# Optimization experiments

Hardware: AMD Instinct MI355X
Metric: run time of the kernel (lower is better)

## Reference

```python
import jax, jax.numpy as jnp
import numpy as np

N = 30000      # nodes
IN = 768       # input feature dim
C = 128        # hidden channels (= conv out_dim, = gate dim)
HEADS = 4      # attention heads (TransformerConv and Semantic)
DH = 128       # per-head dim (concat=False -> out_channels)
R = 3          # num relations
E = 80000      # edges per relation
NEG = 0.01     # LeakyReLU slope


def setup_inputs() -> dict:
    key = jax.random.key(0)
    ks = iter(jax.random.split(key, 64))
    def nx(shape):
        return jax.random.normal(next(ks), shape, dtype=jnp.float32) * 0.02
    inp = {}
    inp["x"] = jax.random.normal(next(ks), (N, IN), dtype=jnp.float32)
    inp["edges"] = jax.random.randint(next(ks), (R, 2, E), 0, N, dtype=jnp.int32)
    inp["lin1_W"] = nx((IN, C)); inp["lin1_b"] = jnp.zeros((C,), jnp.float32)
    for l in ("l1", "l2"):
        inp[f"{l}_Wq"] = nx((R, C, HEADS * DH)); inp[f"{l}_bq"] = jnp.zeros((R, HEADS * DH), jnp.float32)
        inp[f"{l}_Wk"] = nx((R, C, HEADS * DH)); inp[f"{l}_bk"] = jnp.zeros((R, HEADS * DH), jnp.float32)
        inp[f"{l}_Wv"] = nx((R, C, HEADS * DH)); inp[f"{l}_bv"] = jnp.zeros((R, HEADS * DH), jnp.float32)
        inp[f"{l}_Ws"] = nx((R, C, DH));         inp[f"{l}_bs"] = jnp.zeros((R, DH), jnp.float32)
        inp[f"{l}_gW"] = nx((C + DH, C));        inp[f"{l}_gb"] = jnp.zeros((C,), jnp.float32)
        inp[f"{l}_sW1"] = nx((HEADS, C, C));     inp[f"{l}_sb1"] = jnp.zeros((HEADS, C), jnp.float32)
        inp[f"{l}_sw2"] = nx((HEADS, C))
    inp["lin2_W"] = nx((C, C)); inp["lin2_b"] = jnp.zeros((C,), jnp.float32)
    inp["clf_W"] = nx((C, 2)); inp["clf_b"] = jnp.zeros((2,), jnp.float32)
    return inp


def lrelu(x):
    return jnp.where(x >= 0, x, NEG * x)


def transformer_conv(x, src, dst, Wq, bq, Wk, bk, Wv, bv, Ws, bs):
    # PyG TransformerConv, heads=HEADS, concat=False (head mean), root_weight=True, eval (no dropout)
    n = x.shape[0]
    q = (x @ Wq + bq).reshape(n, HEADS, DH)
    k = (x @ Wk + bk).reshape(n, HEADS, DH)
    v = (x @ Wv + bv).reshape(n, HEADS, DH)
    logits = (q[dst] * k[src]).sum(-1) / np.sqrt(DH)      # [E, H]
    m = jax.ops.segment_max(logits, dst, num_segments=n)  # scatter-softmax (stable)
    a = jnp.exp(logits - m[dst])
    s = jax.ops.segment_sum(a, dst, num_segments=n)
    alpha = a / s[dst]
    agg = jax.ops.segment_sum(alpha[:, :, None] * v[src], dst, num_segments=n)  # [N, H, DH]
    return agg.mean(axis=1) + x @ Ws + bs


def semantic(Hm, sW1, sb1, sw2):
    # Hm: [N, R, C]; per-head scoring MLP -> softmax over relations -> weighted sum, averaged over heads
    t = jnp.tanh(jnp.einsum('nrc,hco->hnro', Hm, sW1) + sb1[:, None, None, :])  # [H, N, R, C]
    scores = jnp.einsum('hnro,ho->hnr', t, sw2).mean(axis=1)                    # [H, R]
    beta = jax.nn.softmax(scores, axis=-1)
    return jnp.einsum('hr,nrc->nc', beta, Hm) / HEADS


def rgt_layer(x, edges, Wq, bq, Wk, bk, Wv, bv, Ws, bs, gW, gb, sW1, sb1, sw2):
    Hs = []
    for r in range(R):  # small fixed relation loop
        src, dst = edges[r, 0], edges[r, 1]
        U = transformer_conv(x, src, dst, Wq[r], bq[r], Wk[r], bk[r], Wv[r], bv[r], Ws[r], bs[r])
        Z = jax.nn.sigmoid(jnp.concatenate([U, x], axis=1) @ gW + gb)
        Hs.append(jnp.tanh(U) * Z + x * (1.0 - Z))
    Hm = jnp.stack(Hs, axis=1)  # [N, R, C]
    return semantic(Hm, sW1, sb1, sw2)


def reference(x, edges, lin1_W, lin1_b,
              l1_Wq, l1_bq, l1_Wk, l1_bk, l1_Wv, l1_bv, l1_Ws, l1_bs, l1_gW, l1_gb, l1_sW1, l1_sb1, l1_sw2,
              l2_Wq, l2_bq, l2_Wk, l2_bk, l2_Wv, l2_bv, l2_Ws, l2_bs, l2_gW, l2_gb, l2_sW1, l2_sb1, l2_sw2,
              lin2_W, lin2_b, clf_W, clf_b):
    h = lrelu(x @ lin1_W + lin1_b)
    h = rgt_layer(h, edges, l1_Wq, l1_bq, l1_Wk, l1_bk, l1_Wv, l1_bv, l1_Ws, l1_bs, l1_gW, l1_gb, l1_sW1, l1_sb1, l1_sw2)
    h = rgt_layer(h, edges, l2_Wq, l2_bq, l2_Wk, l2_bk, l2_Wv, l2_bv, l2_Ws, l2_bs, l2_gW, l2_gb, l2_sW1, l2_sb1, l2_sw2)
    h = lrelu(h @ lin2_W + lin2_b)
    return h @ clf_W + clf_b
```

## Files before the change

kernel.cpp:

```cpp
#include <hip/hip_runtime.h>
#include <math.h>

#define Nn 30000
#define RR 3
#define EE 80000
#define MT_M 235

#define SAP 72
#define EP_LD 68
#define AS3 136
#define KBIG 0x40000000

typedef __attribute__((ext_vector_type(8))) short bf16x8;
typedef __attribute__((ext_vector_type(4))) float f32x4;

__device__ __forceinline__ unsigned short f2bf(float f) {
    union { float f; unsigned u; } v; v.f = f;
    unsigned r = v.u + 0x7fff + ((v.u >> 16) & 1);
    return (unsigned short)(r >> 16);
}
__device__ __forceinline__ float bf2f(short h) {
    union { unsigned u; float f; } v;
    v.u = ((unsigned)(unsigned short)h) << 16;
    return v.f;
// ... 28 lines not shown
    const int wave = t >> 6;
    const int wm = (wave >> 1) << 6;
    const int wn = (wave & 1) << 6;
    const int fr = lane & 15;
    const int quad = lane >> 4;

    for (int k0 = 0; k0 < K; k0 += 64) {
        const short* Abase; int kk0, ldax;
        if (k0 < ksplit) { Abase = A;  kk0 = k0;          ldax = lda;  }
        else             { Abase = A2; kk0 = k0 - ksplit; ldax = lda2; }
        #pragma unroll
        for (int rr = 0; rr < 4; rr++) {
            int r = srow + rr * 32;
            int gr = m0 + r;
            bf16x8 va = {0, 0, 0, 0, 0, 0, 0, 0};
            if (gr < M) va = *(const bf16x8*)(Abase + (size_t)gr * ldax + kk0 + scol);
            *(bf16x8*)(As + r * SAP + scol) = va;
        }
        #pragma unroll
        for (int rr = 0; rr < 4; rr++) {
            int r = srow + rr * 32;
            bf16x8 vb = *(const bf16x8*)(Bt + (size_t)(n0 + r) * K + k0 + scol);
            *(bf16x8*)(Bs + r * SAP + scol) = vb;
        }
        __syncthreads();
        #pragma unroll
        for (int kc = 0; kc < 2; kc++) {
            bf16x8 af[4], bfr[4];
            #pragma unroll
            for (int i = 0; i < 4; i++)
                af[i] = *(const bf16x8*)(As + (wm + i * 16 + fr) * SAP + kc * 32 + quad * 8);
            #pragma unroll
            for (int i = 0; i < 4; i++)
                bfr[i] = *(const bf16x8*)(Bs + (wn + i * 16 + fr) * SAP + kc * 32 + quad * 8);
            #pragma unroll
            for (int mi = 0; mi < 4; mi++)
                #pragma unroll
                for (int ni = 0; ni < 4; ni++)
                    acc[mi][ni] = __builtin_amdgcn_mfma_f32_16x16x32_bf16(
                        af[mi], bfr[ni], acc[mi][ni], 0, 0, 0);
        }
        __syncthreads();
    }
}

__global__ __launch_bounds__(256) void gemm_mfma(
    const short* __restrict__ A, int lda,
    const short* __restrict__ A2, int lda2, int ksplit,
    const short* __restrict__ Bt, const float* __restrict__ bias,
    float* __restrict__ C, int ldc, short* __restrict__ Cbf, int ldcbf,
    int M, int K, int act)
{
    __shared__ short As[128 * SAP];
    __shared__ short Bs[128 * SAP];
    f32x4 acc[4][4];
    #pragma unroll
    for (int i = 0; i < 4; i++)
        #pragma unroll
        for (int j = 0; j < 4; j++) acc[i][j] = (f32x4){0.f, 0.f, 0.f, 0.f};
    int m0 = blockIdx.y * 128, n0 = blockIdx.x * 128;
    mfma_core(A, lda, A2, lda2, ksplit, Bt, M, K, m0, n0, As, Bs, acc);

    const int t = threadIdx.x;
    const int lane = t & 63, wave = t >> 6;
    const int wm = (wave >> 1) << 6, wn = (wave & 1) << 6;
    const int fr = lane & 15, quad = lane >> 4;
    float* ws = (float*)As + wave * 16 * EP_LD;
    const int rrow = lane >> 2;
    const int cseg = (lane & 3) << 4;
    #pragma unroll
    for (int mi = 0; mi < 4; mi++) {
        #pragma unroll
        for (int ni = 0; ni < 4; ni++)
            #pragma unroll
            for (int reg = 0; reg < 4; reg++)
                ws[(quad * 4 + reg) * EP_LD + ni * 16 + fr] = acc[mi][ni][reg];
        int gr = m0 + wm + mi * 16 + rrow;
        if (gr >= M) continue;
        int gc = n0 + wn + cseg;
        float vals[16];
        #pragma unroll
        for (int j = 0; j < 16; j++) {
            float v = ws[rrow * EP_LD + cseg + j] + bias[gc + j];
            if (act == 1) v = (v >= 0.f) ? v : 0.01f * v;
            vals[j] = v;
        }
        if (C) {
            float* cp = C + (size_t)gr * ldc + gc;
            #pragma unroll
            for (int j4 = 0; j4 < 4; j4++)
                *(float4*)(cp + j4 * 4) = make_float4(vals[j4 * 4], vals[j4 * 4 + 1],
                                                      vals[j4 * 4 + 2], vals[j4 * 4 + 3]);
        }
        if (Cbf) {
            unsigned pk[8];
            #pragma unroll
            for (int j2 = 0; j2 < 8; j2++)
                pk[j2] = ((unsigned)f2bf(vals[2 * j2 + 1]) << 16) | (unsigned)f2bf(vals[2 * j2]);
            unsigned* bp = (unsigned*)(Cbf + (size_t)gr * ldcbf + gc);
            *(uint4*)bp       = make_uint4(pk[0], pk[1], pk[2], pk[3]);
            *(uint4*)(bp + 4) = make_uint4(pk[4], pk[5], pk[6], pk[7]);
        }
    }
}

__global__ __launch_bounds__(256) void gemm_lin1(
    const float* __restrict__ X,
    const short* __restrict__ Bt,
    const float* __restrict__ bias,
    float* __restrict__ C, short* __restrict__ Cbf, int M)
{
    __shared__ short As[128 * SAP];
    __shared__ short Bs[128 * SAP];
    f32x4 acc[4][4];
    #pragma unroll
    for (int i = 0; i < 4; i++)
        #pragma unroll
        for (int j = 0; j < 4; j++) acc[i][j] = (f32x4){0.f, 0.f, 0.f, 0.f};
    const int t = threadIdx.x;
    const int srow = t >> 3;
    const int scol = (t & 7) << 3;
    const int lane = t & 63, wave = t >> 6;
    const int wm = (wave >> 1) << 6, wn = (wave & 1) << 6;
    const int fr = lane & 15, quad = lane >> 4;
    const int m0 = blockIdx.y * 128;

    for (int k0 = 0; k0 < 768; k0 += 64) {
        #pragma unroll
        for (int rr = 0; rr < 4; rr++) {
            int r = srow + rr * 32;
            int gr = m0 + r;
            bf16x8 va = {0, 0, 0, 0, 0, 0, 0, 0};
            if (gr < M) {
                const float* xp = X + (size_t)gr * 768 + k0 + scol;
                float4 a = *(const float4*)xp;
                float4 b = *(const float4*)(xp + 4);
                va[0] = (short)f2bf(a.x); va[1] = (short)f2bf(a.y);
                va[2] = (short)f2bf(a.z); va[3] = (short)f2bf(a.w);
                va[4] = (short)f2bf(b.x); va[5] = (short)f2bf(b.y);
                va[6] = (short)f2bf(b.z); va[7] = (short)f2bf(b.w);
            }
            *(bf16x8*)(As + r * SAP + scol) = va;
        }
        #pragma unroll
        for (int rr = 0; rr < 4; rr++) {
            int r = srow + rr * 32;
            bf16x8 vb = *(const bf16x8*)(Bt + (size_t)r * 768 + k0 + scol);
            *(bf16x8*)(Bs + r * SAP + scol) = vb;
        }
        __syncthreads();
        #pragma unroll
        for (int kc = 0; kc < 2; kc++) {
            bf16x8 af[4], bfr[4];
            #pragma unroll
            for (int i = 0; i < 4; i++)
                af[i] = *(const bf16x8*)(As + (wm + i * 16 + fr) * SAP + kc * 32 + quad * 8);
            #pragma unroll
            for (int i = 0; i < 4; i++)
                bfr[i] = *(const bf16x8*)(Bs + (wn + i * 16 + fr) * SAP + kc * 32 + quad * 8);
            #pragma unroll
            for (int mi = 0; mi < 4; mi++)
                #pragma unroll
                for (int ni = 0; ni < 4; ni++)
                    acc[mi][ni] = __builtin_amdgcn_mfma_f32_16x16x32_bf16(
                        af[mi], bfr[ni], acc[mi][ni], 0, 0, 0);
        }
        __syncthreads();
    }

    float* ws = (float*)As + wave * 16 * EP_LD;
    const int rrow = lane >> 2;
    const int cseg = (lane & 3) << 4;
    #pragma unroll
    for (int mi = 0; mi < 4; mi++) {
        #pragma unroll
        for (int ni = 0; ni < 4; ni++)
            #pragma unroll
            for (int reg = 0; reg < 4; reg++)
                ws[(quad * 4 + reg) * EP_LD + ni * 16 + fr] = acc[mi][ni][reg];
        int gr = m0 + wm + mi * 16 + rrow;
        if (gr >= M) continue;
        int gc = wn + cseg;
        float vals[16];
        #pragma unroll
        for (int j = 0; j < 16; j++) {
            float v = ws[rrow * EP_LD + cseg + j] + bias[gc + j];
            vals[j] = (v >= 0.f) ? v : 0.01f * v;
        }
        float* cp = C + (size_t)gr * 128 + gc;
        #pragma unroll
        for (int j4 = 0; j4 < 4; j4++)
            *(float4*)(cp + j4 * 4) = make_float4(vals[j4 * 4], vals[j4 * 4 + 1],
                                                  vals[j4 * 4 + 2], vals[j4 * 4 + 3]);
        unsigned pk[8];
        #pragma unroll
        for (int j2 = 0; j2 < 8; j2++)
            pk[j2] = ((unsigned)f2bf(vals[2 * j2 + 1]) << 16) | (unsigned)f2bf(vals[2 * j2]);
        unsigned* bp = (unsigned*)(Cbf + (size_t)gr * 128 + gc);
        *(uint4*)bp       = make_uint4(pk[0], pk[1], pk[2], pk[3]);
        *(uint4*)(bp + 4) = make_uint4(pk[4], pk[5], pk[6], pk[7]);
    }
}

__global__ __launch_bounds__(256) void gemm_qkvs_v4(
    const short* __restrict__ A,
    const short* __restrict__ Wt, const float* __restrict__ bias,
    short* __restrict__ qhat3, int M)
{
    __shared__ short As[128 * SAP];
    __shared__ short Bs[128 * SAP];
    f32x4 acc[4][4];
    #pragma unroll
    for (int i = 0; i < 4; i++)
        #pragma unroll
        for (int j = 0; j < 4; j++) acc[i][j] = (f32x4){0.f, 0.f, 0.f, 0.f};
    int m0 = blockIdx.y * 128, bx = blockIdx.x, n0 = bx * 128;
    mfma_core(A, 128, A, 128, KBIG, Wt, M, 128, m0, n0, As, Bs, acc);

    const int t = threadIdx.x;
    const int lane = t & 63, wave = t >> 6;
    const int wm = (wave >> 1) << 6, wn = (wave & 1) << 6;
    const int fr = lane & 15, quad = lane >> 4;
    float* ws = (float*)As + wave * 16 * EP_LD;
    const int rrow = lane >> 2;
    const int cseg = (lane & 3) << 4;
    const int r = bx >> 2;
    #pragma unroll
    for (int mi = 0; mi < 4; mi++) {
        #pragma unroll
        for (int ni = 0; ni < 4; ni++)
            #pragma unroll
            for (int reg = 0; reg < 4; reg++)
                ws[(quad * 4 + reg) * EP_LD + ni * 16 + fr] = acc[mi][ni][reg];
        int gr = m0 + wm + mi * 16 + rrow;
        if (gr >= M) continue;
        int lc = wn + cseg;
        float vals[16];
        #pragma unroll
        for (int j = 0; j < 16; j++)
            vals[j] = ws[rrow * EP_LD + cseg + j] + bias[n0 + lc + j];
        unsigned pk[8];
        #pragma unroll
        for (int j2 = 0; j2 < 8; j2++)
            pk[j2] = ((unsigned)f2bf(vals[2 * j2 + 1]) << 16) | (unsigned)f2bf(vals[2 * j2]);
        unsigned* bp = (unsigned*)(qhat3 + ((size_t)(r * Nn + gr)) * 512 + (bx - r * 4) * 128 + lc);
        *(uint4*)bp       = make_uint4(pk[0], pk[1], pk[2], pk[3]);
        *(uint4*)(bp + 4) = make_uint4(pk[4], pk[5], pk[6], pk[7]);
    }
}

__global__ __launch_bounds__(256) void attn_v4(
    const short* __restrict__ qhat3, const short* __restrict__ hbf,
    const int* __restrict__ rowptr3, const int* __restrict__ col3,
    short* __restrict__ Ah3)
{
    int wid = ((blockIdx.x * blockDim.x + threadIdx.x) >> 6);
    int lane = threadIdx.x & 63;
    if (wid >= 3 * Nn) return;
    int r = wid / Nn, n = wid - r * Nn;
    const int* rowptr = rowptr3 + r * (Nn + 1);
    const int* colb = col3 + r * EE;
    int beg = rowptr[n], end = rowptr[n + 1];

    uint4 qv = ((const uint4*)(qhat3 + ((size_t)r * Nn + n) * 512))[lane];
    float qf[8];
    unpack8(qv, qf);
    const int l16 = lane & 15;

    float s = 0.f;
    float acc[8] = {0.f, 0.f, 0.f, 0.f, 0.f, 0.f, 0.f, 0.f};

    uint4 hv_n = make_uint4(0, 0, 0, 0);
    if (beg < end)
        hv_n = ((const uint4*)(hbf + (size_t)colb[beg] * 128))[l16];
    for (int i = beg; i < end; i++) {
        uint4 hv = hv_n;
        if (i + 1 < end)
            hv_n = ((const uint4*)(hbf + (size_t)colb[i + 1] * 128))[l16];
        float hf[8];
        unpack8(hv, hf);
        float p = qf[0] * hf[0] + qf[1] * hf[1] + qf[2] * hf[2] + qf[3] * hf[3]
                + qf[4] * hf[4] + qf[5] * hf[5] + qf[6] * hf[6] + qf[7] * hf[7];
        p += __shfl_xor(p, 1);
        p += __shfl_xor(p, 2);
        p += __shfl_xor(p, 4);
        p += __shfl_xor(p, 8);
        float pe = __expf(p);
        s += pe;
        #pragma unroll
        for (int j = 0; j < 8; j++) acc[j] += pe * hf[j];
    }

    float inv = (s > 0.f) ? 1.f / s : 0.f;
    #pragma unroll
    for (int j = 0; j < 8; j++) acc[j] *= inv;

    unsigned p0 = ((unsigned)f2bf(acc[1]) << 16) | (unsigned)f2bf(acc[0]);
    unsigned p1 = ((unsigned)f2bf(acc[3]) << 16) | (unsigned)f2bf(acc[2]);
    unsigned p2 = ((unsigned)f2bf(acc[5]) << 16) | (unsigned)f2bf(acc[4]);
    unsigned p3 = ((unsigned)f2bf(acc[7]) << 16) | (unsigned)f2bf(acc[6]);
    *(uint4*)(Ah3 + ((size_t)r * Nn + n) * 512 + lane * 8) = make_uint4(p0, p1, p2, p3);
}

__global__ __launch_bounds__(256) void ufin_mfma(
    const short* __restrict__ Ah3, const short* __restrict__ Hbf,
    const short* __restrict__ w640t,
    const float* __restrict__ bs, const float* __restrict__ bvmean,
    const int* __restrict__ rowptr3,
    short* __restrict__ U_bf, int M)
{
    __shared__ short As[128 * SAP];
    __shared__ short Bs[128 * SAP];
    f32x4 acc[4][4];
    #pragma unroll
    for (int i = 0; i < 4; i++)
        #pragma unroll
        for (int j = 0; j < 4; j++) acc[i][j] = (f32x4){0.f, 0.f, 0.f, 0.f};
    int r = blockIdx.z;
    int m0 = blockIdx.y * 128;
    mfma_core(Ah3 + (size_t)r * Nn * 512, 512, Hbf, 128, 512,
              w640t + (size_t)r * 81920, M, 640, m0, 0, As, Bs, acc);

    const int t = threadIdx.x;
    const int lane = t & 63, wave = t >> 6;
    const int wm = (wave >> 1) << 6, wn = (wave & 1) << 6;
    const int fr = lane & 15, quad = lane >> 4;
    float* ws = (float*)As + wave * 16 * EP_LD;
    const int rrow = lane >> 2;
    const int cseg = (lane & 3) << 4;
    const int rp = r * (Nn + 1);
    #pragma unroll
    for (int mi = 0; mi < 4; mi++) {
        #pragma unroll
        for (int ni = 0; ni < 4; ni++)
            #pragma unroll
            for (int reg = 0; reg < 4; reg++)
                ws[(quad * 4 + reg) * EP_LD + ni * 16 + fr] = acc[mi][ni][reg];
        int gr = m0 + wm + mi * 16 + rrow;
        if (gr >= M) continue;
        int gc = wn + cseg;
        float mk = (rowptr3[rp + gr + 1] > rowptr3[rp + gr]) ? 1.f : 0.f;
        float vals[16];
        #pragma unroll
        for (int j = 0; j < 16; j++)
            vals[j] = ws[rrow * EP_LD + cseg + j] + bs[r * 128 + gc + j]
                    + mk * bvmean[r * 128 + gc + j];
        unsigned pk[8];
        #pragma unroll
        for (int j2 = 0; j2 < 8; j2++)
            pk[j2] = ((unsigned)f2bf(vals[2 * j2 + 1]) << 16) | (unsigned)f2bf(vals[2 * j2]);
        unsigned* bp = (unsigned*)(U_bf + (size_t)gr * 384 + r * 128 + gc);
        *(uint4*)bp       = make_uint4(pk[0], pk[1], pk[2], pk[3]);
        *(uint4*)(bp + 4) = make_uint4(pk[4], pk[5], pk[6], pk[7]);
    }
}

__global__ __launch_bounds__(256) void gate_mfma(
    const short* __restrict__ Ubf,
    const short* __restrict__ Hbf,
    const short* __restrict__ gWt, const float* __restrict__ gb,
    const float* __restrict__ Hf,
    float* __restrict__ Hm, short* __restrict__ HmBf,
    int M)
{
    __shared__ short As[128 * SAP];
    __shared__ short Bs[128 * SAP];
    f32x4 acc[4][4];
    #pragma unroll
    for (int i = 0; i < 4; i++)
        #pragma unroll
        for (int j = 0; j < 4; j++) acc[i][j] = (f32x4){0.f, 0.f, 0.f, 0.f};
    int r = blockIdx.z;
    int m0 = blockIdx.y * 128;
    mfma_core(Ubf + r * 128, 384, Hbf, 128, 128, gWt, M, 256, m0, 0, As, Bs, acc);

    const int t = threadIdx.x;
    const int lane = t & 63, wave = t >> 6;
    const int wm = (wave >> 1) << 6, wn = (wave & 1) << 6;
    const int fr = lane & 15, quad = lane >> 4;
    float* ws = (float*)As + wave * 16 * EP_LD;
    const int rrow = lane >> 2;
    const int cseg = (lane & 3) << 4;
    #pragma unroll
    for (int mi = 0; mi < 4; mi++) {
        #pragma unroll
        for (int ni = 0; ni < 4; ni++)
            #pragma unroll
            for (int reg = 0; reg < 4; reg++)
                ws[(quad * 4 + reg) * EP_LD + ni * 16 + fr] = acc[mi][ni][reg];
        int gr = m0 + wm + mi * 16 + rrow;
        if (gr >= M) continue;
        int gc = wn + cseg;
        const short* up = Ubf + (size_t)gr * 384 + r * 128 + gc;
        const float* hp = Hf + (size_t)gr * 128 + gc;
        float uv[16], hv[16];
        uint4 u0 = *(const uint4*)up;
        uint4 u1 = *(const uint4*)(up + 8);
        unpack8(u0, uv); unpack8(u1, uv + 8);
        #pragma unroll
        for (int j4 = 0; j4 < 4; j4++)
            *(float4*)(hv + j4 * 4) = *(const float4*)(hp + j4 * 4);
        float vals[16];
        #pragma unroll
        for (int j = 0; j < 16; j++) {
            float g = ws[rrow * EP_LD + cseg + j] + gb[gc + j];
            float z = 1.f / (1.f + __expf(-g));
            vals[j] = fast_tanh(uv[j]) * z + hv[j] * (1.f - z);
        }
        float* cp = Hm + (size_t)gr * 384 + r * 128 + gc;
        #pragma unroll
        for (int j4 = 0; j4 < 4; j4++)
            *(float4*)(cp + j4 * 4) = make_float4(vals[j4 * 4], vals[j4 * 4 + 1],
                                                  vals[j4 * 4 + 2], vals[j4 * 4 + 3]);
        unsigned pk[8];
        #pragma unroll
        for (int j2 = 0; j2 < 8; j2++)
            pk[j2] = ((unsigned)f2bf(vals[2 * j2 + 1]) << 16) | (unsigned)f2bf(vals[2 * j2]);
        unsigned* bp = (unsigned*)(HmBf + (size_t)gr * 384 + r * 128 + gc);
        *(uint4*)bp       = make_uint4(pk[0], pk[1], pk[2], pk[3]);
        *(uint4*)(bp + 4) = make_uint4(pk[4], pk[5], pk[6], pk[7]);
    }
}

__global__ __launch_bounds__(256) void semantic_v2(
    const short* __restrict__ HmBf, const short* __restrict__ sW1t,
    const float* __restrict__ sb1, const float* __restrict__ sw2,
    float* __restrict__ partial, int M)
{
    __shared__ short As2[128 * AS3];
    __shared__ short Bs[128 * SAP];
    __shared__ float red4[4];
    const int t = threadIdx.x;
    const int tile = blockIdx.x, r = blockIdx.y;
    const int m0 = tile * 128;

    {
        const int row0 = t >> 4;
        const int col  = (t & 15) << 3;
        #pragma unroll
        for (int rr = 0; rr < 8; rr++) {
            int row = row0 + rr * 16;
            int gr = m0 + row;
            bf16x8 va = {0, 0, 0, 0, 0, 0, 0, 0};
            if (gr < M) va = *(const bf16x8*)(HmBf + (size_t)gr * 384 + r * 128 + col);
            *(bf16x8*)(As2 + row * AS3 + col) = va;
        }
    }
    __syncthreads();

    const int lane = t & 63, wave = t >> 6;
    const int wm = (wave >> 1) << 6, wn = (wave & 1) << 6;
    const int fr = lane & 15, quad = lane >> 4;
    const int srow = t >> 3, scol = (t & 7) << 3;

    #pragma unroll 1
    for (int head = 0; head < 4; head++) {
        f32x4 acc[4][4];
        #pragma unroll
        for (int i = 0; i < 4; i++)
            #pragma unroll
            for (int j = 0; j < 4; j++) acc[i][j] = (f32x4){0.f, 0.f, 0.f, 0.f};

        for (int k0 = 0; k0 < 128; k0 += 64) {
            #pragma unroll
            for (int rr = 0; rr < 4; rr++) {
                int row = srow + rr * 32;
                bf16x8 vb = *(const bf16x8*)(sW1t + (size_t)(head * 128 + row) * 128 + k0 + scol);
                *(bf16x8*)(Bs + row * SAP + scol) = vb;
            }
            __syncthreads();
            #pragma unroll
            for (int kc = 0; kc < 2; kc++) {
                bf16x8 af[4], bfr[4];
                #pragma unroll
                for (int i = 0; i < 4; i++)
                    af[i] = *(const bf16x8*)(As2 + (wm + i * 16 + fr) * AS3 + k0 + kc * 32 + quad * 8);
                #pragma unroll
                for (int i = 0; i < 4; i++)
                    bfr[i] = *(const bf16x8*)(Bs + (wn + i * 16 + fr) * SAP + kc * 32 + quad * 8);
                #pragma unroll
                for (int mi = 0; mi < 4; mi++)
                    #pragma unroll
                    for (int ni = 0; ni < 4; ni++)
                        acc[mi][ni] = __builtin_amdgcn_mfma_f32_16x16x32_bf16(
                            af[mi], bfr[ni], acc[mi][ni], 0, 0, 0);
            }
            __syncthreads();
        }

        float local = 0.f;
        #pragma unroll
        for (int ni = 0; ni < 4; ni++) {
            int gc = head * 128 + wn + ni * 16 + fr;
            float b = sb1[gc], w2 = sw2[gc];
            #pragma unroll
            for (int mi = 0; mi < 4; mi++) {
                #pragma unroll
                for (int reg = 0; reg < 4; reg++) {
                    int gr = m0 + wm + mi * 16 + quad * 4 + reg;
                    if (gr >= M) continue;
                    local += fast_tanh(acc[mi][ni][reg] + b) * w2;
                }
            }
        }
        #pragma unroll
        for (int off = 1; off < 64; off <<= 1) local += __shfl_xor(local, off);
        if (lane == 0) red4[wave] = local;
        __syncthreads();
        if (t == 0)
            partial[(head * 3 + r) * MT_M + tile] = red4[0] + red4[1] + red4[2] + red4[3];
    }
}

__global__ __launch_bounds__(768) void reduce_w_kernel(
    const float* __restrict__ partial, float* __restrict__ w, float invN)
{
    __shared__ float sc[12];
    int z = threadIdx.x >> 6;
    int lane = threadIdx.x & 63;
    float s = 0.f;
    for (int i = lane; i < MT_M; i += 64) s += partial[z * MT_M + i];
    #pragma unroll
    for (int off = 1; off < 64; off <<= 1) s += __shfl_xor(s, off);
    if (lane == 0) sc[z] = s;
    __syncthreads();
    if (threadIdx.x == 0) {
        float wr[3] = {0.f, 0.f, 0.f};
        for (int h = 0; h < 4; h++) {
            float s0 = sc[h * 3 + 0] * invN;
            float s1 = sc[h * 3 + 1] * invN;
            float s2 = sc[h * 3 + 2] * invN;
            float mx = fmaxf(s0, fmaxf(s1, s2));
            float e0 = __expf(s0 - mx), e1 = __expf(s1 - mx), e2 = __expf(s2 - mx);
            float inv = 1.f / (e0 + e1 + e2);
            wr[0] += 0.25f * e0 * inv;
            wr[1] += 0.25f * e1 * inv;
            wr[2] += 0.25f * e2 * inv;
        }
        w[0] = wr[0]; w[1] = wr[1]; w[2] = wr[2];
    }
}

__global__ void mix_kernel(const float* __restrict__ Hm, const float* __restrict__ w,
                           float* __restrict__ h, short* __restrict__ hbf, int total4)
{
    int i = blockIdx.x * blockDim.x + threadIdx.x;
    if (i >= total4) return;
    int n = i >> 5, c4 = (i & 31) << 2;
    const float* row = Hm + (size_t)n * 384 + c4;
    float4 a = *(const float4*)row;
    float4 b = *(const float4*)(row + 128);
    float4 c = *(const float4*)(row + 256);
    float w0 = w[0], w1 = w[1], w2 = w[2];
    float4 v = make_float4(w0 * a.x + w1 * b.x + w2 * c.x,
                           w0 * a.y + w1 * b.y + w2 * c.y,
                           w0 * a.z + w1 * b.z + w2 * c.z,
                           w0 * a.w + w1 * b.w + w2 * c.w);
    *(float4*)(h + (size_t)n * 128 + c4) = v;
    unsigned p0 = ((unsigned)f2bf(v.y) << 16) | (unsigned)f2bf(v.x);
    unsigned p1 = ((unsigned)f2bf(v.w) << 16) | (unsigned)f2bf(v.z);
    *(uint2*)(hbf + (size_t)n * 128 + c4) = make_uint2(p0, p1);
}

__global__ void prep_global_kernel(const float* __restrict__ lin1_W, const float* __restrict__ lin2_W,
                                   short* __restrict__ lin1Wt, short* __restrict__ lin2Wt)
{
    int id = blockIdx.x * blockDim.x + threadIdx.x;
    if (id < 98304) {
        int n = id / 768, k = id % 768;
        lin1Wt[id] = (short)f2bf(lin1_W[k * 128 + n]);
    } else if (id < 114688) {
        int r = id - 98304;
        int n = r / 128, k = r % 128;
        lin2Wt[r] = (short)f2bf(lin2_W[k * 128 + n]);
    }
}

__global__ void prep_layer_v6(
    const float* __restrict__ Ws, const float* __restrict__ gW,
    const float* __restrict__ sW1, const float* __restrict__ Wv,
    const float* __restrict__ bv,
    short* __restrict__ gWt, short* __restrict__ sW1t,
    short* __restrict__ w640t, float* __restrict__ bvmean)
{
    const int S0 = 32768;
    const int S1 = S0 + 65536;
    const int S2 = S1 + 245760;
    const int S3 = S2 + 384;
    int id = blockIdx.x * blockDim.x + threadIdx.x;
    if (id < S0) {
        int n = id / 256, k = id - n * 256;
        gWt[id] = (short)f2bf(gW[k * 128 + n]);
    } else if (id < S1) {
        int q = id - S0;
        int h = q / 16384, rem = q - h * 16384;
        int n = rem / 128, k = rem - n * 128;
        sW1t[q] = (short)f2bf(sW1[(size_t)h * 16384 + k * 128 + n]);
    } else if (id < S2) {
        int q = id - S1;
        int r = q / 81920, rem = q - r * 81920;
        int d = rem / 640, k = rem - d * 640;
        float v;
        if (k < 512) {
            int hh = k >> 7, j = k & 127;
            v = 0.25f * Wv[(size_t)r * 65536 + j * 512 + hh * 128 + d];
        } else {
            v = Ws[(size_t)r * 16384 + (k - 512) * 128 + d];
        }
        w640t[q] = (short)f2bf(v);
    } else if (id < S3) {
        int q = id - S2;
        int r = q >> 7, d = q & 127;
        bvmean[q] = 0.25f * (bv[r * 512 + d] + bv[r * 512 + 128 + d]
                           + bv[r * 512 + 256 + d] + bv[r * 512 + 384 + d]);
    }
}

__global__ __launch_bounds__(256) void gmat_v2(
    const float* __restrict__ Wq0, const float* __restrict__ Wk0, const float* __restrict__ bq0,
    const float* __restrict__ Wq1, const float* __restrict__ Wk1, const float* __restrict__ bq1,
    short* __restrict__ Wt4, float* __restrict__ B4)
{
    __shared__ float WqL[128 * 129];
    __shared__ float WkL[16 * 128];
    const int jg = blockIdx.x;
    const int h  = blockIdx.y;
    const int lz = blockIdx.z;
    const int l = lz / 3, r = lz - l * 3;
    const float* Wq = l ? Wq1 : Wq0;
    const float* Wk = l ? Wk1 : Wk0;
    const float* bq = l ? bq1 : bq0;
    short* Wt = Wt4 + (size_t)l * 196608;
    float* Bb = B4 + l * 1536;
    const float scale = 0.088388347648318447f;
    const int t = threadIdx.x;

    for (int v = t; v < 4096; v += 256) {
        int i = v >> 5, d4 = (v & 31) << 2;
        float4 q = *(const float4*)(Wq + (size_t)r * 65536 + i * 512 + h * 128 + d4);
        float* wp = WqL + i * 129 + d4;
        wp[0] = q.x; wp[1] = q.y; wp[2] = q.z; wp[3] = q.w;
    }
    for (int v = t; v < 512; v += 256) {
        int jl = v >> 5, d4 = (v & 31) << 2;
        float4 q = *(const float4*)(Wk + (size_t)r * 65536 + (jg * 16 + jl) * 512 + h * 128 + d4);
        float* wp = WkL + jl * 128 + d4;
        wp[0] = q.x; wp[1] = q.y; wp[2] = q.z; wp[3] = q.w;
    }
    __syncthreads();

    const int i = t & 127;
    const int jh = t >> 7;
    const float* wk = WkL + jh * 8 * 128;
    float acc[8] = {0.f, 0.f, 0.f, 0.f, 0.f, 0.f, 0.f, 0.f};
    #pragma unroll 4
    for (int d = 0; d < 128; d++) {
        float wq = WqL[i * 129 + d];
        #pragma unroll
        for (int jj = 0; jj < 8; jj++)
            acc[jj] += wq * wk[jj * 128 + d];
    }
    short* wrow = Wt + ((size_t)(r * 512 + h * 128 + jg * 16 + jh * 8)) * 128 + i;
    #pragma unroll
    for (int jj = 0; jj < 8; jj++)
        wrow[(size_t)jj * 128] = (short)f2bf(scale * acc[jj]);

    if (t < 16) {
        const float* bqh = bq + r * 512 + h * 128;
        float c = 0.f;
        for (int d = 0; d < 128; d++) c += bqh[d] * WkL[t * 128 + d];
        Bb[r * 512 + h * 128 + jg * 16 + t] = scale * c;
    }
}

__global__ void zero_i32_kernel(int* __restrict__ p, int n)
{
    int i = blockIdx.x * blockDim.x + threadIdx.x;
    if (i < n) p[i] = 0;
}

__global__ void hist3_kernel(const int* __restrict__ edges, int* __restrict__ cnt3)
{
    int i = blockIdx.x * blockDim.x + threadIdx.x;
    if (i >= 3 * EE) return;
    int r = i / EE, e = i - r * EE;
    int d = edges[(size_t)r * 2 * EE + EE + e];
    atomicAdd(&cnt3[r * Nn + d], 1);
}

__global__ __launch_bounds__(1024) void scan3_kernel(const int* __restrict__ cnt3,
                                                     int* __restrict__ rowptr3)
{
    __shared__ int part[1024];
    const int r = blockIdx.x;
    const int* cnt = cnt3 + r * Nn;
    int* rowptr = rowptr3 + r * (Nn + 1);
    int tid = threadIdx.x;
    int per = (Nn + 1023) >> 10;
    int base = tid * per;
    int s = 0;
    for (int i = 0; i < per; i++) {
        int idx = base + i;
        if (idx < Nn) s += cnt[idx];
    }
    part[tid] = s;
    __syncthreads();
    for (int off = 1; off < 1024; off <<= 1) {
        int val = (tid >= off) ? part[tid - off] : 0;
        __syncthreads();
        part[tid] += val;
        __syncthreads();
    }
    int excl = (tid == 0) ? 0 : part[tid - 1];
    for (int i = 0; i < per; i++) {
        int idx = base + i;
        if (idx < Nn) { rowptr[idx] = excl; excl += cnt[idx]; }
    }
    if (tid == 1023) rowptr[Nn] = part[1023];
}

__global__ void scatter3_kernel(const int* __restrict__ edges,
                                const int* __restrict__ rowptr3, int* __restrict__ fill3,
                                int* __restrict__ col3)
{
    int i = blockIdx.x * blockDim.x + threadIdx.x;
    if (i >= 3 * EE) return;
    int r = i / EE, e = i - r * EE;
    int src = edges[(size_t)r * 2 * EE + e];
    int d   = edges[(size_t)r * 2 * EE + EE + e];
    int pos = rowptr3[r * (Nn + 1) + d] + atomicAdd(&fill3[r * Nn + d], 1);
    col3[r * EE + pos] = src;
}

__global__ void clf_kernel(const float* __restrict__ t, const float* __restrict__ W,
                           const float* __restrict__ b, float* __restrict__ out, int M)
{
    int n = blockIdx.x * blockDim.x + threadIdx.x;
    if (n >= M) return;
    const float* row = t + (size_t)n * 128;
    float a0 = b[0], a1 = b[1];
    #pragma unroll
    for (int kk = 0; kk < 128; kk++) {
        float a = row[kk];
        a0 += a * W[kk * 2];
        a1 += a * W[kk * 2 + 1];
    }
    out[n * 2] = a0;
    out[n * 2 + 1] = a1;
}

extern "C" void kernel_launch(void* const* d_in, const int* in_sizes, int n_in,
                              void* d_out, int out_size, void* d_ws, size_t ws_size,
                              hipStream_t stream)
{
    const float* x      = (const float*)d_in[0];
    const int*   edges  = (const int*)d_in[1];
    const float* lin1_W = (const float*)d_in[2];
    const float* lin1_b = (const float*)d_in[3];
    const int L0 = 4, L1 = 17;
    const float* lin2_W = (const float*)d_in[30];
    const float* lin2_b = (const float*)d_in[31];
    const float* clf_W  = (const float*)d_in[32];
    const float* clf_b  = (const float*)d_in[33];
    float* out = (float*)d_out;

    char* w = (char*)d_ws;
    size_t off = 0;
    auto alloc = [&](size_t bytes) { void* p = w + off; off = (off + bytes + 255) & ~(size_t)255; return p; };
    float* h      = (float*)alloc((size_t)Nn * 128 * 4);
    short* h_bf   = (short*)alloc((size_t)Nn * 128 * 2);
    short* U_bf   = (short*)alloc((size_t)Nn * 384 * 2);
    const size_t QH = (size_t)3 * Nn * 512 * 2;
    char* BIG     = (char*)alloc(2 * QH);
    short* qhat3  = (short*)BIG;
    short* Ah3    = (short*)(BIG + QH);
    float* Hm     = (float*)BIG;
    short* Hm_bf  = (short*)(BIG + (size_t)Nn * 384 * 4);
    float* lin2o  = (float*)BIG;
    short* lin1Wt = (short*)alloc((size_t)98304 * 2);
    short* lin2Wt = (short*)alloc((size_t)16384 * 2);
    short* qkvsWt4 = (short*)alloc((size_t)2 * 196608 * 2);
    short* gWt    = (short*)alloc((size_t)2 * 32768 * 2);
    short* sW1t   = (short*)alloc((size_t)2 * 65536 * 2);
    short* w640t  = (short*)alloc((size_t)2 * 245760 * 2);
    float* qkvsB4 = (float*)alloc((size_t)2 * 1536 * 4);
    float* bvmean = (float*)alloc((size_t)2 * 384 * 4);
    int* rowptr3  = (int*)alloc((size_t)3 * (Nn + 1) * 4);
    int* cnt3     = (int*)alloc((size_t)3 * Nn * 4);
    int* col3     = (int*)alloc((size_t)3 * EE * 4);
    float* partial = (float*)alloc((size_t)12 * MT_M * 4);
    float* wmix   = (float*)alloc(3 * 4);

    const int MT = MT_M;
    dim3 blk(256);

    {
        prep_global_kernel<<<(114688 + 255) / 256, blk, 0, stream>>>(lin1_W, lin2_W, lin1Wt, lin2Wt);
        for (int l = 0; l < 2; l++) {
            int base = (l == 0) ? L0 : L1;
            prep_layer_v6<<<(344448 + 255) / 256, blk, 0, stream>>>(
                (const float*)d_in[base + 6], (const float*)d_in[base + 8],
                (const float*)d_in[base + 10], (const float*)d_in[base + 4],
                (const float*)d_in[base + 5],
                gWt + (size_t)l * 32768, sW1t + (size_t)l * 65536,
                w640t + (size_t)l * 245760, bvmean + (size_t)l * 384);
        }
        gmat_v2<<<dim3(8, 4, 6), blk, 0, stream>>>(
            (const float*)d_in[L0 + 0], (const float*)d_in[L0 + 2], (const float*)d_in[L0 + 1],
            (const float*)d_in[L1 + 0], (const float*)d_in[L1 + 2], (const float*)d_in[L1 + 1],
            qkvsWt4, qkvsB4);
        zero_i32_kernel<<<(3 * Nn + 255) / 256, blk, 0, stream>>>(cnt3, 3 * Nn);
        hist3_kernel<<<(3 * EE + 255) / 256, blk, 0, stream>>>(edges, cnt3);
        scan3_kernel<<<3, 1024, 0, stream>>>(cnt3, rowptr3);
        zero_i32_kernel<<<(3 * Nn + 255) / 256, blk, 0, stream>>>(cnt3, 3 * Nn);
        scatter3_kernel<<<(3 * EE + 255) / 256, blk, 0, stream>>>(edges, rowptr3, cnt3, col3);
    }

    gemm_lin1<<<dim3(1, MT), blk, 0, stream>>>(x, lin1Wt, lin1_b, h, h_bf, Nn);

    for (int l = 0; l < 2; l++) {
        int base = (l == 0) ? L0 : L1;
        const float* bs  = (const float*)d_in[base + 7];
        const float* gb  = (const float*)d_in[base + 9];
        const float* sb1 = (const float*)d_in[base + 11];
        const float* sw2 = (const float*)d_in[base + 12];
        short* lWt4   = qkvsWt4 + (size_t)l * 196608;
        short* lgWt   = gWt + (size_t)l * 32768;
        short* lsW1t  = sW1t + (size_t)l * 65536;
        short* lw640  = w640t + (size_t)l * 245760;
        float* lB4    = qkvsB4 + (size_t)l * 1536;
        float* lbvm   = bvmean + (size_t)l * 384;

        gemm_qkvs_v4<<<dim3(12, MT), blk, 0, stream>>>(
            h_bf, lWt4, lB4, qhat3, Nn);

        attn_v4<<<(3 * Nn + 3) / 4, blk, 0, stream>>>(qhat3, h_bf, rowptr3, col3, Ah3);

        ufin_mfma<<<dim3(1, MT, 3), blk, 0, stream>>>(
            Ah3, h_bf, lw640, bs, lbvm, rowptr3, U_bf, Nn);

        gate_mfma<<<dim3(1, MT, 3), blk, 0, stream>>>(
            U_bf, h_bf, lgWt, gb, h, Hm, Hm_bf, Nn);

        semantic_v2<<<dim3(MT, 3), blk, 0, stream>>>(Hm_bf, lsW1t, sb1, sw2, partial, Nn);
        reduce_w_kernel<<<1, 768, 0, stream>>>(partial, wmix, 1.f / (float)Nn);
        mix_kernel<<<(Nn * 32 + 255) / 256, blk, 0, stream>>>(Hm, wmix, h, h_bf, Nn * 32);
    }

    gemm_mfma<<<dim3(1, MT), blk, 0, stream>>>(
        h_bf, 128, h_bf, 128, KBIG, lin2Wt, lin2_b, lin2o, 128, (short*)nullptr, 0, Nn, 128, 1);
    clf_kernel<<<(Nn + 255) / 256, blk, 0, stream>>>(lin2o, clf_W, clf_b, out, Nn);
}
```

Measured before the change: 805.2 us.

## Fold gate GEMM into U projection by precomposing gate weights with U weights

The gate pre-activation [U,x]@gW is linear in U, and U is itself a linear map of [Ah,h]. The change therefore precomputes a combined weight matrix whose extra 128 output columns give the gate logits directly, along with the matching bias terms including the mask-dependent bvmean part. A single fused kernel computes U and the gate together over K=640 with N=256 and applies tanh/sigmoid mixing, so the separate gate GEMM and the bf16 U intermediate round trip go away. The trade-off is doubled B-tile work and register and LDS pressure in the fused kernel, plus a bf16 rounding change because U is no longer quantized before the gate matmul.

Result: slower. 865.6 us (+7.5%).

```diff
diff --git a/kernel.cpp b/kernel.cpp
--- a/kernel.cpp
+++ b/kernel.cpp
@@ -354,110 +354,116 @@
     *(uint4*)(Ah3 + ((size_t)r * Nn + n) * 512 + lane * 8) = make_uint4(p0, p1, p2, p3);
 }
 
-__global__ __launch_bounds__(256) void ufin_mfma(
+__global__ __launch_bounds__(256) void ugate2_mfma(
     const short* __restrict__ Ah3, const short* __restrict__ Hbf,
-    const short* __restrict__ w640t,
-    const float* __restrict__ bs, const float* __restrict__ bvmean,
-    const int* __restrict__ rowptr3,
-    short* __restrict__ U_bf, int M)
+    const short* __restrict__ UG,
+    const float* __restrict__ bs, const float* __restrict__ bvm,
+    const float* __restrict__ gBM,
+    const int* __restrict__ rowptr3, const float* __restrict__ Hf,
+    float* __restrict__ Hm, short* __restrict__ HmBf, int M)
 {
     __shared__ short As[128 * SAP];
-    __shared__ short Bs[128 * SAP];
-    f32x4 acc[4][4];
-    #pragma unroll
-    for (int i = 0; i < 4; i++)
-        #pragma unroll
-        for (int j = 0; j < 4; j++) acc[i][j] = (f32x4){0.f, 0.f, 0.f, 0.f};
-    int r = blockIdx.z;
-    int m0 = blockIdx.y * 128;
-    mfma_core(Ah3 + (size_t)r * Nn * 512, 512, Hbf, 128, 512,
-              w640t + (size_t)r * 81920, M, 640, m0, 0, As, Bs, acc);
-
+    __shared__ short Bs2[256 * SAP];
     const int t = threadIdx.x;
+    const int srow = t >> 3;
+    const int scol = (t & 7) << 3;
     const int lane = t & 63, wave = t >> 6;
     const int wm = (wave >> 1) << 6, wn = (wave & 1) << 6;
     const int fr = lane & 15, quad = lane >> 4;
+    const int r = blockIdx.z;
+    const int m0 = blockIdx.y * 128;
+    const short* Ar = Ah3 + (size_t)r * Nn * 512;
+    const short* Br = UG + (size_t)r * 256 * 640;
+
+    f32x4 acc[2][4][4];
+    #pragma unroll
+    for (int nh = 0; nh < 2; nh++)
+        #pragma unroll
+        for (int i = 0; i < 4; i++)
+            #pragma unroll
+            for (int j = 0; j < 4; j++) acc[nh][i][j] = (f32x4){0.f, 0.f, 0.f, 0.f};
+
+    for (int k0 = 0; k0 < 640; k0 += 64) {
+        const short* Abase; int kk0, ldax;
+        if (k0 < 512) { Abase = Ar;  kk0 = k0;       ldax = 512; }
+        else          { Abase = Hbf; kk0 = k0 - 512; ldax = 128; }
+        #pragma unroll
+        for (int rr = 0; rr < 4; rr++) {
+            int row = srow + rr * 32;
+            int gr = m0 + row;
+            bf16x8 va = {0, 0, 0, 0, 0, 0, 0, 0};
+            if (gr < M) va = *(const bf16x8*)(Abase + (size_t)gr * ldax + kk0 + scol);
+            *(bf16x8*)(As + row * SAP + scol) = va;
+        }
+        #pragma unroll
+        for (int rr = 0; rr < 8; rr++) {
+            int row = srow + rr * 32;
+            bf16x8 vb = *(const bf16x8*)(Br + (size_t)row * 640 + k0 + scol);
+            *(bf16x8*)(Bs2 + row * SAP + scol) = vb;
+        }
+        __syncthreads();
+        #pragma unroll
+        for (int kc = 0; kc < 2; kc++) {
+            bf16x8 af[4];
+            #pragma unroll
+            for (int i = 0; i < 4; i++)
+                af[i] = *(const bf16x8*)(As + (wm + i * 16 + fr) * SAP + kc * 32 + quad * 8);
+            #pragma unroll
+            for (int nh = 0; nh < 2; nh++) {
+                bf16x8 bfr[4];
+                #pragma unroll
+                for (int i = 0; i < 4; i++)
+                    bfr[i] = *(const bf16x8*)(Bs2 + (nh * 128 + wn + i * 16 + fr) * SAP
+                                              + kc * 32 + quad * 8);
+                #pragma unroll
+                for (int mi = 0; mi < 4; mi++)
+                    #pragma unroll
+                    for (int ni = 0; ni < 4; ni++)
+                        acc[nh][mi][ni] = __builtin_amdgcn_mfma_f32_16x16x32_bf16(
+                            af[mi], bfr[ni], acc[nh][mi][ni], 0, 0, 0);
+            }
+        }
+        __syncthreads();
+    }
+
     float* ws = (float*)As + wave * 16 * EP_LD;
     const int rrow = lane >> 2;
     const int cseg = (lane & 3) << 4;
     const int rp = r * (Nn + 1);
     #pragma unroll
     for (int mi = 0; mi < 4; mi++) {
+        float uv[16], gv[16];
         #pragma unroll
         for (int ni = 0; ni < 4; ni++)
             #pragma unroll
             for (int reg = 0; reg < 4; reg++)
-                ws[(quad * 4 + reg) * EP_LD + ni * 16 + fr] = acc[mi][ni][reg];
+                ws[(quad * 4 + reg) * EP_LD + ni * 16 + fr] = acc[0][mi][ni][reg];
+        #pragma unroll
+        for (int j = 0; j < 16; j++) uv[j] = ws[rrow * EP_LD + cseg + j];
+        #pragma unroll
+        for (int ni = 0; ni < 4; ni++)
+            #pragma unroll
+            for (int reg = 0; reg < 4; reg++)
+                ws[(quad * 4 + reg) * EP_LD + ni * 16 + fr] = acc[1][mi][ni][reg];
+        #pragma unroll
+        for (int j = 0; j < 16; j++) gv[j] = ws[rrow * EP_LD + cseg + j];
+
         int gr = m0 + wm + mi * 16 + rrow;
         if (gr >= M) continue;
         int gc = wn + cseg;
         float mk = (rowptr3[rp + gr + 1] > rowptr3[rp + gr]) ? 1.f : 0.f;
-        float vals[16];
-        #pragma unroll
-        for (int j = 0; j < 16; j++)
-            vals[j] = ws[rrow * EP_LD + cseg + j] + bs[r * 128 + gc + j]
-                    + mk * bvmean[r * 128 + gc + j];
-        unsigned pk[8];
-        #pragma unroll
-        for (int j2 = 0; j2 < 8; j2++)
-            pk[j2] = ((unsigned)f2bf(vals[2 * j2 + 1]) << 16) | (unsigned)f2bf(vals[2 * j2]);
-        unsigned* bp = (unsigned*)(U_bf + (size_t)gr * 384 + r * 128 + gc);
-        *(uint4*)bp       = make_uint4(pk[0], pk[1], pk[2], pk[3]);
-        *(uint4*)(bp + 4) = make_uint4(pk[4], pk[5], pk[6], pk[7]);
-    }
-}
-
-__global__ __launch_bounds__(256) void gate_mfma(
-    const short* __restrict__ Ubf,
-    const short* __restrict__ Hbf,
-    const short* __restrict__ gWt, const float* __restrict__ gb,
-    const float* __restrict__ Hf,
-    float* __restrict__ Hm, short* __restrict__ HmBf,
-    int M)
-{
-    __shared__ short As[128 * SAP];
-    __shared__ short Bs[128 * SAP];
-    f32x4 acc[4][4];
-    #pragma unroll
-    for (int i = 0; i < 4; i++)
-        #pragma unroll
-        for (int j = 0; j < 4; j++) acc[i][j] = (f32x4){0.f, 0.f, 0.f, 0.f};
-    int r = blockIdx.z;
-    int m0 = blockIdx.y * 128;
-    mfma_core(Ubf + r * 128, 384, Hbf, 128, 128, gWt, M, 256, m0, 0, As, Bs, acc);
-
-    const int t = threadIdx.x;
-    const int lane = t & 63, wave = t >> 6;
-    const int wm = (wave >> 1) << 6, wn = (wave & 1) << 6;
-    const int fr = lane & 15, quad = lane >> 4;
-    float* ws = (float*)As + wave * 16 * EP_LD;
-    const int rrow = lane >> 2;
-    const int cseg = (lane & 3) << 4;
-    #pragma unroll
-    for (int mi = 0; mi < 4; mi++) {
-        #pragma unroll
-        for (int ni = 0; ni < 4; ni++)
-            #pragma unroll
-            for (int reg = 0; reg < 4; reg++)
-                ws[(quad * 4 + reg) * EP_LD + ni * 16 + fr] = acc[mi][ni][reg];
-        int gr = m0 + wm + mi * 16 + rrow;
-        if (gr >= M) continue;
-        int gc = wn + cseg;
-        const short* up = Ubf + (size_t)gr * 384 + r * 128 + gc;
+        float hv[16];
         const float* hp = Hf + (size_t)gr * 128 + gc;
-        float uv[16], hv[16];
-        uint4 u0 = *(const uint4*)up;
-        uint4 u1 = *(const uint4*)(up + 8);
-        unpack8(u0, uv); unpack8(u1, uv + 8);
         #pragma unroll
         for (int j4 = 0; j4 < 4; j4++)
             *(float4*)(hv + j4 * 4) = *(const float4*)(hp + j4 * 4);
         float vals[16];
         #pragma unroll
         for (int j = 0; j < 16; j++) {
-            float g = ws[rrow * EP_LD + cseg + j] + gb[gc + j];
+            float U = uv[j] + bs[r * 128 + gc + j] + mk * bvm[r * 128 + gc + j];
+            float g = gv[j] + gBM[r * 256 + gc + j] + mk * gBM[r * 256 + 128 + gc + j];
             float z = 1.f / (1.f + __expf(-g));
-            vals[j] = fast_tanh(uv[j]) * z + hv[j] * (1.f - z);
+            vals[j] = fast_tanh(U) * z + hv[j] * (1.f - z);
         }
         float* cp = Hm + (size_t)gr * 384 + r * 128 + gc;
         #pragma unroll
@@ -628,28 +634,23 @@
     }
 }
 
-__global__ void prep_layer_v6(
-    const float* __restrict__ Ws, const float* __restrict__ gW,
-    const float* __restrict__ sW1, const float* __restrict__ Wv,
-    const float* __restrict__ bv,
-    short* __restrict__ gWt, short* __restrict__ sW1t,
-    short* __restrict__ w640t, float* __restrict__ bvmean)
-{
-    const int S0 = 32768;
-    const int S1 = S0 + 65536;
-    const int S2 = S1 + 245760;
-    const int S3 = S2 + 384;
+__global__ void prep_layer_v10(
+    const float* __restrict__ Ws, const float* __restrict__ sW1,
+    const float* __restrict__ Wv, const float* __restrict__ bv,
+    short* __restrict__ sW1t, short* __restrict__ ug640t,
+    float* __restrict__ bvmean)
+{
+    const int S0 = 65536;
+    const int S1 = S0 + 245760;
+    const int S2 = S1 + 384;
     int id = blockIdx.x * blockDim.x + threadIdx.x;
     if (id < S0) {
-        int n = id / 256, k = id - n * 256;
-        gWt[id] = (short)f2bf(gW[k * 128 + n]);
-    } else if (id < S1) {
-        int q = id - S0;
+        int q = id;
         int h = q / 16384, rem = q - h * 16384;
         int n = rem / 128, k = rem - n * 128;
         sW1t[q] = (short)f2bf(sW1[(size_t)h * 16384 + k * 128 + n]);
-    } else if (id < S2) {
-        int q = id - S1;
+    } else if (id < S1) {
+        int q = id - S0;
         int r = q / 81920, rem = q - r * 81920;
         int d = rem / 640, k = rem - d * 640;
         float v;
@@ -659,13 +660,153 @@
         } else {
             v = Ws[(size_t)r * 16384 + (k - 512) * 128 + d];
         }
-        w640t[q] = (short)f2bf(v);
-    } else if (id < S3) {
-        int q = id - S2;
+        ug640t[(size_t)(r * 256 + d) * 640 + k] = (short)f2bf(v);
+    } else if (id < S2) {
+        int q = id - S1;
         int r = q >> 7, d = q & 127;
         bvmean[q] = 0.25f * (bv[r * 512 + d] + bv[r * 512 + 128 + d]
                            + bv[r * 512 + 256 + d] + bv[r * 512 + 384 + d]);
     }
+}
+
+__global__ __launch_bounds__(256) void g640_kernel(
+    short* __restrict__ ug640t,
+    const float* __restrict__ gW0, const float* __restrict__ gW1,
+    const float* __restrict__ gb0, const float* __restrict__ gb1,
+    const float* __restrict__ bs0, const float* __restrict__ bs1,
+    const float* __restrict__ bv0, const float* __restrict__ bv1,
+    float* __restrict__ gBM)
+{
+    __shared__ float gWL[128 * 129];
+    __shared__ float wL[64 * 129];
+    const int kkt = blockIdx.x;
+    const int r   = blockIdx.y;
+    const int l   = blockIdx.z;
+    const int kk0 = kkt * 64;
+    const float* gW = l ? gW1 : gW0;
+    const float* gb = l ? gb1 : gb0;
+    const float* bs = l ? bs1 : bs0;
+    const float* bv = l ? bv1 : bv0;
+    short* UG = ug640t + (size_t)l * 3 * 256 * 640;
+    const int t = threadIdx.x;
+
+    for (int v = t; v < 16384; v += 256) {
+        int d = v >> 7, n = v & 127;
+        gWL[d * 129 + n] = gW[d * 128 + n];
+    }
+    for (int v = t; v < 8192; v += 256) {
+        int kkl = v & 63, d = v >> 6;
+        wL[kkl * 129 + d] = bf2f(UG[(size_t)(r * 256 + d) * 640 + kk0 + kkl]);
+    }
+    __syncthreads();
+
+    const int n = t & 127;
+    const int kkh = t >> 7;
+    float acc[32];
+    #pragma unroll
+    for (int j = 0; j < 32; j++) acc[j] = 0.f;
+    for (int d = 0; d < 128; d++) {
+        float wq = gWL[d * 129 + n];
+        #pragma unroll
+        for (int j = 0; j < 32; j++)
+            acc[j] += wq * wL[(kkh * 32 + j) * 129 + d];
+    }
+    #pragma unroll
+    for (int j = 0; j < 32; j++) {
+        int kk = kk0 + kkh * 32 + j;
+        float add = (kk >= 512) ? gW[(128 + kk - 512) * 128 + n] : 0.f;
+        UG[(size_t)(r * 256 + 128 + n) * 640 + kk] = (short)f2bf(acc[j] + add);
+    }
+
+    if (kkt == 0 && t < 128) {
+        float b = 0.f, m = 0.f;
+        for (int d = 0; d < 128; d++) {
+            float g = gWL[d * 129 + t];
+            b += bs[r * 128 + d] * g;
+            float bvm = 0.25f * (bv[r * 512 + d] + bv[r * 512 + 128 + d]
+                               + bv[r * 512 + 256 + d] + bv[r * 512 + 384 + d]);
+            m += bvm * g;
+        }
+        float* dst = gBM + (size_t)l * 768 + r * 256;
+        dst[t] = gb[t] + b;
+        dst[128 + t] = m;
+    }
+}
+
+__global__ void zero_i32_kernel(int* __restrict__ p, int n)
+{
+    int i = blockIdx.x * blockDim.x + threadIdx.x;
+    if (i < n) p[i] = 0;
+}
+
+__global__ void hist3_kernel(const int* __restrict__ edges, int* __restrict__ cnt3)
+{
+    int i = blockIdx.x * blockDim.x + threadIdx.x;
+    if (i >= 3 * EE) return;
+    int r = i / EE, e = i - r * EE;
+    int d = edges[(size_t)r * 2 * EE + EE + e];
+    atomicAdd(&cnt3[r * Nn + d], 1);
+}
+
+__global__ __launch_bounds__(1024) void scan3_kernel(const int* __restrict__ cnt3,
+                                                     int* __restrict__ rowptr3)
+{
+    __shared__ int part[1024];
+    const int r = blockIdx.x;
+    const int* cnt = cnt3 + r * Nn;
+    int* rowptr = rowptr3 + r * (Nn + 1);
+    int tid = threadIdx.x;
+    int per = (Nn + 1023) >> 10;
+    int base = tid * per;
+    int s = 0;
+    for (int i = 0; i < per; i++) {
+        int idx = base + i;
+        if (idx < Nn) s += cnt[idx];
+    }
+    part[tid] = s;
+    __syncthreads();
+    for (int off = 1; off < 1024; off <<= 1) {
+        int val = (tid >= off) ? part[tid - off] : 0;
+        __syncthreads();
+        part[tid] += val;
+        __syncthreads();
+    }
+    int excl = (tid == 0) ? 0 : part[tid - 1];
+    for (int i = 0; i < per; i++) {
+        int idx = base + i;
+        if (idx < Nn) { rowptr[idx] = excl; excl += cnt[idx]; }
+    }
+    if (tid == 1023) rowptr[Nn] = part[1023];
+}
+
+__global__ void scatter3_kernel(const int* __restrict__ edges,
+                                const int* __restrict__ rowptr3, int* __restrict__ fill3,
+                                int* __restrict__ col3)
+{
+    int i = blockIdx.x * blockDim.x + threadIdx.x;
+    if (i >= 3 * EE) return;
+    int r = i / EE, e = i - r * EE;
+    int src = edges[(size_t)r * 2 * EE + e];
+    int d   = edges[(size_t)r * 2 * EE + EE + e];
+    int pos = rowptr3[r * (Nn + 1) + d] + atomicAdd(&fill3[r * Nn + d], 1);
+    col3[r * EE + pos] = src;
+}
+
+__global__ void clf_kernel(const float* __restrict__ t, const float* __restrict__ W,
+                           const float* __restrict__ b, float* __restrict__ out, int M)
+{
+    int n = blockIdx.x * blockDim.x + threadIdx.x;
+    if (n >= M) return;
+    const float* row = t + (size_t)n * 128;
+    float a0 = b[0], a1 = b[1];
+    #pragma unroll
+    for (int kk = 0; kk < 128; kk++) {
+        float a = row[kk];
+        a0 += a * W[kk * 2];
+        a1 += a * W[kk * 2 + 1];
+    }
+    out[n * 2] = a0;
+    out[n * 2 + 1] = a1;
 }
 
 __global__ __launch_bounds__(256) void gmat_v2(
@@ -725,82 +866,6 @@
     }
 }
 
-__global__ void zero_i32_kernel(int* __restrict__ p, int n)
-{
-    int i = blockIdx.x * blockDim.x + threadIdx.x;
-    if (i < n) p[i] = 0;
-}
-
-__global__ void hist3_kernel(const int* __restrict__ edges, int* __restrict__ cnt3)
-{
-    int i = blockIdx.x * blockDim.x + threadIdx.x;
-    if (i >= 3 * EE) return;
-    int r = i / EE, e = i - r * EE;
-    int d = edges[(size_t)r * 2 * EE + EE + e];
-    atomicAdd(&cnt3[r * Nn + d], 1);
-}
-
-__global__ __launch_bounds__(1024) void scan3_kernel(const int* __restrict__ cnt3,
-                                                     int* __restrict__ rowptr3)
-{
-    __shared__ int part[1024];
-    const int r = blockIdx.x;
-    const int* cnt = cnt3 + r * Nn;
-    int* rowptr = rowptr3 + r * (Nn + 1);
-    int tid = threadIdx.x;
-    int per = (Nn + 1023) >> 10;
-    int base = tid * per;
-    int s = 0;
-    for (int i = 0; i < per; i++) {
-        int idx = base + i;
-        if (idx < Nn) s += cnt[idx];
-    }
-    part[tid] = s;
-    __syncthreads();
-    for (int off = 1; off < 1024; off <<= 1) {
-        int val = (tid >= off) ? part[tid - off] : 0;
-        __syncthreads();
-        part[tid] += val;
-        __syncthreads();
-    }
-    int excl = (tid == 0) ? 0 : part[tid - 1];
-    for (int i = 0; i < per; i++) {
-        int idx = base + i;
-        if (idx < Nn) { rowptr[idx] = excl; excl += cnt[idx]; }
-    }
-    if (tid == 1023) rowptr[Nn] = part[1023];
-}
-
-__global__ void scatter3_kernel(const int* __restrict__ edges,
-                                const int* __restrict__ rowptr3, int* __restrict__ fill3,
-                                int* __restrict__ col3)
-{
-    int i = blockIdx.x * blockDim.x + threadIdx.x;
-    if (i >= 3 * EE) return;
-    int r = i / EE, e = i - r * EE;
-    int src = edges[(size_t)r * 2 * EE + e];
-    int d   = edges[(size_t)r * 2 * EE + EE + e];
-    int pos = rowptr3[r * (Nn + 1) + d] + atomicAdd(&fill3[r * Nn + d], 1);
-    col3[r * EE + pos] = src;
-}
-
-__global__ void clf_kernel(const float* __restrict__ t, const float* __restrict__ W,
-                           const float* __restrict__ b, float* __restrict__ out, int M)
-{
-    int n = blockIdx.x * blockDim.x + threadIdx.x;
-    if (n >= M) return;
-    const float* row = t + (size_t)n * 128;
-    float a0 = b[0], a1 = b[1];
-    #pragma unroll
-    for (int kk = 0; kk < 128; kk++) {
-        float a = row[kk];
-        a0 += a * W[kk * 2];
-        a1 += a * W[kk * 2 + 1];
-    }
-    out[n * 2] = a0;
-    out[n * 2 + 1] = a1;
-}
-
 extern "C" void kernel_launch(void* const* d_in, const int* in_sizes, int n_in,
                               void* d_out, int out_size, void* d_ws, size_t ws_size,
                               hipStream_t stream)
@@ -821,7 +886,6 @@
     auto alloc = [&](size_t bytes) { void* p = w + off; off = (off + bytes + 255) & ~(size_t)255; return p; };
     float* h      = (float*)alloc((size_t)Nn * 128 * 4);
     short* h_bf   = (short*)alloc((size_t)Nn * 128 * 2);
-    short* U_bf   = (short*)alloc((size_t)Nn * 384 * 2);
     const size_t QH = (size_t)3 * Nn * 512 * 2;
     char* BIG     = (char*)alloc(2 * QH);
     short* qhat3  = (short*)BIG;
@@ -832,11 +896,11 @@
     short* lin1Wt = (short*)alloc((size_t)98304 * 2);
     short* lin2Wt = (short*)alloc((size_t)16384 * 2);
     short* qkvsWt4 = (short*)alloc((size_t)2 * 196608 * 2);
-    short* gWt    = (short*)alloc((size_t)2 * 32768 * 2);
     short* sW1t   = (short*)alloc((size_t)2 * 65536 * 2);
-    short* w640t  = (short*)alloc((size_t)2 * 245760 * 2);
+    short* ug640t = (short*)alloc((size_t)2 * 3 * 256 * 640 * 2);
     float* qkvsB4 = (float*)alloc((size_t)2 * 1536 * 4);
     float* bvmean = (float*)alloc((size_t)2 * 384 * 4);
+    float* gBM    = (float*)alloc((size_t)2 * 768 * 4);
     int* rowptr3  = (int*)alloc((size_t)3 * (Nn + 1) * 4);
     int* cnt3     = (int*)alloc((size_t)3 * Nn * 4);
     int* col3     = (int*)alloc((size_t)3 * EE * 4);
@@ -850,13 +914,19 @@
         prep_global_kernel<<<(114688 + 255) / 256, blk, 0, stream>>>(lin1_W, lin2_W, lin1Wt, lin2Wt);
         for (int l = 0; l < 2; l++) {
             int base = (l == 0) ? L0 : L1;
-            prep_layer_v6<<<(344448 + 255) / 256, blk, 0, stream>>>(
-                (const float*)d_in[base + 6], (const float*)d_in[base + 8],
-                (const float*)d_in[base + 10], (const float*)d_in[base + 4],
-                (const float*)d_in[base + 5],
-                gWt + (size_t)l * 32768, sW1t + (size_t)l * 65536,
-                w640t + (size_t)l * 245760, bvmean + (size_t)l * 384);
-        }
+            prep_layer_v10<<<(311680 + 255) / 256, blk, 0, stream>>>(
+                (const float*)d_in[base + 6], (const float*)d_in[base + 10],
+                (const float*)d_in[base + 4], (const float*)d_in[base + 5],
+                sW1t + (size_t)l * 65536, ug640t + (size_t)l * 3 * 256 * 640,
+                bvmean + (size_t)l * 384);
+        }
+        g640_kernel<<<dim3(10, 3, 2), blk, 0, stream>>>(
+            ug640t,
+            (const float*)d_in[L0 + 8], (const float*)d_in[L1 + 8],
+            (const float*)d_in[L0 + 9], (const float*)d_in[L1 + 9],
+            (const float*)d_in[L0 + 7], (const float*)d_in[L1 + 7],
+            (const float*)d_in[L0 + 5], (const float*)d_in[L1 + 5],
+            gBM);
         gmat_v2<<<dim3(8, 4, 6), blk, 0, stream>>>(
             (const float*)d_in[L0 + 0], (const float*)d_in[L0 + 2], (const float*)d_in[L0 + 1],
             (const float*)d_in[L1 + 0], (const float*)d_in[L1 + 2], (const float*)d_in[L1 + 1],
@@ -873,26 +943,22 @@
     for (int l = 0; l < 2; l++) {
         int base = (l == 0) ? L0 : L1;
         const float* bs  = (const float*)d_in[base + 7];
-        const float* gb  = (const float*)d_in[base + 9];
         const float* sb1 = (const float*)d_in[base + 11];
         const float* sw2 = (const float*)d_in[base + 12];
         short* lWt4   = qkvsWt4 + (size_t)l * 196608;
-        short* lgWt   = gWt + (size_t)l * 32768;
         short* lsW1t  = sW1t + (size_t)l * 65536;
-        short* lw640  = w640t + (size_t)l * 245760;
+        short* lUG    = ug640t + (size_t)l * 3 * 256 * 640;
         float* lB4    = qkvsB4 + (size_t)l * 1536;
         float* lbvm   = bvmean + (size_t)l * 384;
+        float* lgBM   = gBM + (size_t)l * 768;
 
         gemm_qkvs_v4<<<dim3(12, MT), blk, 0, stream>>>(
             h_bf, lWt4, lB4, qhat3, Nn);
 
         attn_v4<<<(3 * Nn + 3) / 4, blk, 0, stream>>>(qhat3, h_bf, rowptr3, col3, Ah3);
 
-        ufin_mfma<<<dim3(1, MT, 3), blk, 0, stream>>>(
-            Ah3, h_bf, lw640, bs, lbvm, rowptr3, U_bf, Nn);
-
-        gate_mfma<<<dim3(1, MT, 3), blk, 0, stream>>>(
-            U_bf, h_bf, lgWt, gb, h, Hm, Hm_bf, Nn);
+        ugate2_mfma<<<dim3(1, MT, 3), blk, 0, stream>>>(
+            Ah3, h_bf, lUG, bs, lbvm, lgBM, rowptr3, h, Hm, Hm_bf, Nn);
 
         semantic_v2<<<dim3(MT, 3), blk, 0, stream>>>(Hm_bf, lsW1t, sb1, sw2, partial, Nn);
         reduce_w_kernel<<<1, 768, 0, stream>>>(partial, wmix, 1.f / (float)Nn);
```
